# Optimization experiments

Hardware: AMD Instinct MI355X
Metric: run time of the kernel (lower is better)

## Reference

```python
import math
import jax, jax.numpy as jnp
import numpy as np

N_WL = 262144
T_REF = 273.15          # CONSTANTS.STANDARD_TEMPERATURE [K]
P_REF = 101325.0        # CONSTANTS.STANDARD_PRESSURE [Pa]
C_LIGHT = 2.99792458e8  # CONSTANTS.SPEED_OF_LIGHT
K_B = 1.380649e-23      # CONSTANTS.BOLTZMANN
N_AVO = 6.02214076e23   # CONSTANTS.AVOGADRO

# hard-coded line database: [center_wl, strength, width, temp_exp]; rows 0-2 O3, 3-5 H2O, 6-9 CO2
LINES = np.array([
    [254.0, 1.15e-17, 2.0, 0.05], [280.0, 5e-18, 3.0, 0.04], [310.0, 1.9e-19, 2.5, 0.03],
    [940.0, 2.5e-23, 3.0, 0.4],  [1130.0, 8.2e-24, 2.5, 0.35], [1380.0, 1.8e-22, 4.0, 0.45],
    [1400.0, 3.5e-25, 3.0, 0.5], [1600.0, 7.8e-26, 2.5, 0.48], [2000.0, 4.2e-24, 4.0, 0.52],
    [2700.0, 1.2e-24, 3.5, 0.49]], dtype=np.float32)
MASS = np.array([48.0]*3 + [18.0]*3 + [44.0]*4, dtype=np.float32)


def setup_inputs() -> dict:
    key = jax.random.key(0)
    ks = jax.random.split(key, 8)
    inp = {
        'wavelengths': jnp.linspace(200.0, 3000.0, N_WL, dtype=jnp.float32),
        'temperature': jnp.float32(250.0),
        'pressure': jnp.float32(80000.0),
        'conc_o3': jnp.float32(1e-6),
        'conc_h2o': jnp.float32(1e-2),
        'conc_co2': jnp.float32(4e-4),
        'mix_w1': jax.random.normal(ks[0], (10, 64), jnp.float32) * 0.3,
        'mix_b1': jnp.zeros((64,), jnp.float32),
        'mix_w2': jax.random.normal(ks[1], (64, 64), jnp.float32) * 0.12,
        'mix_b2': jnp.zeros((64,), jnp.float32),
        'mix_w3': jax.random.normal(ks[2], (64, N_WL), jnp.float32) * 0.12,
        'mix_b3': jnp.zeros((N_WL,), jnp.float32),
        'cont_w1': jax.random.normal(ks[3], (5, 32), jnp.float32) * 0.4,
        'cont_b1': jnp.zeros((32,), jnp.float32),
        'cont_w2': jax.random.normal(ks[4], (32, N_WL), jnp.float32) * 0.17,
        'cont_b2': jnp.zeros((N_WL,), jnp.float32),
    }
    return inp


def _voigt(wl, nu0, gamma_L, gamma_D):
    # wl: [N]; nu0, gamma_L, gamma_D: [L] -> returns [L, N]
    sigma = gamma_D / (math.sqrt(2.0 * math.log(2.0)) + 1e-12)          # [L]
    x = (wl[None, :] - nu0[:, None]) / (sigma[:, None] + 1e-12)          # [L,N]
    y = (gamma_L / (sigma + 1e-12))[:, None]                             # [L,1]
    t = y - 1j * x
    s = jnp.abs(x) + y
    mask1 = s >= 15.0
    mask2 = (s < 15.0) & (jnp.abs(x) >= 5.5)
    w1 = (t * 0.5641896 / (0.5 + t ** 2)).real
    u = t ** 2
    w2 = (t * (1.410474 + u * 0.5641896) / (0.75 + u * (3.0 + u))).real
    w3 = (jnp.exp(-x ** 2) * jnp.cos(2.0 * x * y) / math.sqrt(math.pi)
          + 2.0 * y / math.pi * jnp.sin(x ** 2) / (x ** 2 + y ** 2 + 1e-10))
    result = jnp.where(mask1, w1, jnp.where(mask2, w2, w3))
    return result / (sigma[:, None] * math.sqrt(math.pi) + 1e-12)


def reference(wavelengths, temperature, pressure, conc_o3, conc_h2o, conc_co2,
              mix_w1, mix_b1, mix_w2, mix_b2, mix_w3, mix_b3,
              cont_w1, cont_b1, cont_w2, cont_b2):
    lines = jnp.asarray(LINES)
    mass = jnp.asarray(MASS)
    conc = jnp.stack([conc_o3, conc_o3, conc_o3,
                      conc_h2o, conc_h2o, conc_h2o,
                      conc_co2, conc_co2, conc_co2, conc_co2])          # [10]
    nu0, strength, width, temp_exp = lines[:, 0], lines[:, 1], lines[:, 2], lines[:, 3]
    strength_T = strength * (T_REF / (temperature + 1e-12)) ** temp_exp  # [10]
    gamma_L = width * (pressure / (P_REF + 1e-12)) * jnp.sqrt(T_REF / (temperature + 1e-12))
    gamma_D = nu0 / C_LIGHT * jnp.sqrt(2.0 * K_B * temperature * N_AVO / (mass + 1e-12))

    profiles = _voigt(wavelengths, nu0, gamma_L, gamma_D)                # [10,N]
    cross = jnp.sum((conc * strength_T)[:, None] * profiles, axis=0)     # [N]

    # continuum net: 5 -> 32 (SiLU) -> N (softplus)
    cont_feat = jnp.stack([temperature / (T_REF + 1e-12),
                           pressure / (P_REF + 1e-12),
                           conc_h2o,
                           jnp.float32(1.0), jnp.float32(0.0)])
    h = jax.nn.silu(cont_feat @ cont_w1 + cont_b1)
    continuum = jax.nn.softplus(h @ cont_w2 + cont_b2)
    cross = cross + continuum

    # line-mixing net: 10 -> 64 (SiLU) -> 64 (SiLU) -> N (sigmoid); dropout is eval-mode identity
    mix_feat = jnp.concatenate([jnp.stack([temperature / (T_REF + 1e-12),
                                           pressure / (P_REF + 1e-12)]),
                                cross[:8]])
    m = jax.nn.silu(mix_feat @ mix_w1 + mix_b1)
    m = jax.nn.silu(m @ mix_w2 + mix_b2)
    mixing = jax.nn.sigmoid(m @ mix_w3 + mix_b3)
    return cross * (1.0 + 0.1 * (mixing - 0.5))
```

## Files before the change

### kernel.cpp

```cpp
#include <hip/hip_runtime.h>
#include <math.h>

#define N_WL 262144

#define T_REF 273.15
#define P_REF 101325.0
#define C_LIGHT 299792458.0
#define K_B 1.380649e-23
#define N_AVO 6.02214076e+23

__constant__ float c_nu0[10]  = {254.0f, 280.0f, 310.0f, 940.0f, 1130.0f, 1380.0f, 1400.0f, 1600.0f, 2000.0f, 2700.0f};
__constant__ float c_str[10]  = {1.15e-17f, 5e-18f, 1.9e-19f, 2.5e-23f, 8.2e-24f, 1.8e-22f, 3.5e-25f, 7.8e-26f, 4.2e-24f, 1.2e-24f};
__constant__ float c_wid[10]  = {2.0f, 3.0f, 2.5f, 3.0f, 2.5f, 4.0f, 3.0f, 2.5f, 4.0f, 3.5f};
__constant__ float c_texp[10] = {0.05f, 0.04f, 0.03f, 0.4f, 0.35f, 0.45f, 0.5f, 0.48f, 0.52f, 0.49f};
__constant__ float c_mass[10] = {48.f, 48.f, 48.f, 18.f, 18.f, 18.f, 44.f, 44.f, 44.f, 44.f};
__constant__ int   c_cidx[10] = {0, 0, 0, 1, 1, 1, 2, 2, 2, 2};

#define WS_M2    0
#define WS_H     64
#define WS_NU0   96
#define WS_ISIG  106
#define WS_Y     116
#define WS_SCALE 126
#define WS_TOT   136

__device__ __forceinline__ float siluf(float x)     { return x / (1.0f + __expf(-x)); }
__device__ __forceinline__ float sigmoidf(float x)  { return 1.0f / (1.0f + __expf(-x)); }
__device__ __forceinline__ float softplusf(float x) { return fmaxf(x, 0.0f) + log1pf(expf(-fabsf(x))); }

__device__ __forceinline__ float voigt_w(float x, float y) {
    float ax = fabsf(x);
    float s  = ax + y;
    if (s >= 15.0f) {
        float ur = y * y - x * x;
        float ui = -2.0f * x * y;
        float dr = 0.5f + ur, di = ui;
        float nr = 0.5641896f * y, ni = 0.5641896f * (-x);
        float den = dr * dr + di * di;
        return (nr * dr + ni * di) / den;
    } else if (ax >= 5.5f) {
        float ur = y * y - x * x;
        float ui = -2.0f * x * y;
        float pr = 1.410474f + 0.5641896f * ur;
        float pi_ = 0.5641896f * ui;
        float tr = y, ti = -x;
        float nr = tr * pr - ti * pi_;
        float ni = tr * pi_ + ti * pr;
        float u2r = ur * ur - ui * ui;
        float u2i = 2.0f * ur * ui;
        float dr = 0.75f + 3.0f * ur + u2r;
        float di = 3.0f * ui + u2i;
        float den = dr * dr + di * di;
        return (nr * dr + ni * di) / den;
    } else {
        float x2 = x * x;
        return expf(-x2) * cosf(2.0f * x * y) * 0.5641895835477563f
             + (2.0f * y / 3.14159265358979f) * sinf(x2) / (x2 + y * y + 1e-10f);
    }
}

__global__ void GasAbs_setup_kernel(
    const float* __restrict__ wl,
    const float* __restrict__ Tp, const float* __restrict__ Pp,
    const float* __restrict__ o3, const float* __restrict__ h2o, const float* __restrict__ co2,
    const float* __restrict__ mix_w1, const float* __restrict__ mix_b1,
    const float* __restrict__ mix_w2, const float* __restrict__ mix_b2,
    const float* __restrict__ cont_w1, const float* __restrict__ cont_b1,
    const float* __restrict__ cont_w2, const float* __restrict__ cont_b2,
    float* __restrict__ ws)
{
    __shared__ float sp[WS_TOT];
    __shared__ float s_feat[10];
    __shared__ float s_m1[64];

    const int t = threadIdx.x;
    const double T = (double)Tp[0];
    const double P = (double)Pp[0];
    const float  cc[3] = {o3[0], h2o[0], co2[0]};

    if (t < 10) {
        double nu0 = (double)c_nu0[t];
        double sT  = (double)c_str[t] * pow(T_REF / (T + 1e-12), (double)c_texp[t]);
        double gL  = (double)c_wid[t] * (P / (P_REF + 1e-12)) * sqrt(T_REF / (T + 1e-12));
        double gD  = nu0 / C_LIGHT * sqrt(2.0 * K_B * T * N_AVO / ((double)c_mass[t] + 1e-12));
        double sig = gD / (sqrt(2.0 * log(2.0)) + 1e-12);
        sp[WS_NU0  + t] = (float)nu0;
        sp[WS_ISIG + t] = (float)(1.0 / (sig + 1e-12));
        sp[WS_Y    + t] = (float)(gL / (sig + 1e-12));
        sp[WS_SCALE+ t] = (float)((double)cc[c_cidx[t]] * sT / (sig * sqrt(M_PI) + 1e-12));
    }
    if (t < 32) {
        float cf[5];
        cf[0] = (float)(T / (T_REF + 1e-12));
        cf[1] = (float)(P / (P_REF + 1e-12));
        cf[2] = cc[1];
        cf[3] = 1.0f;
        cf[4] = 0.0f;
        float a = cont_b1[t];
        #pragma unroll
        for (int k = 0; k < 5; k++) a += cf[k] * cont_w1[k * 32 + t];
        sp[WS_H + t] = siluf(a);
    }
    __syncthreads();

    if (t < 8) {
        float w = wl[t];
        float c = cont_b2[t];
        #pragma unroll
        for (int j = 0; j < 32; j++) c += sp[WS_H + j] * cont_w2[(size_t)j * N_WL + t];
        float cross = softplusf(c);
        #pragma unroll
        for (int l = 0; l < 10; l++) {
            float x = (w - sp[WS_NU0 + l]) * sp[WS_ISIG + l];
            cross += sp[WS_SCALE + l] * voigt_w(x, sp[WS_Y + l]);
        }
        s_feat[2 + t] = cross;
    }
    if (t == 0) {
        s_feat[0] = (float)(T / (T_REF + 1e-12));
        s_feat[1] = (float)(P / (P_REF + 1e-12));
    }
    __syncthreads();

    {
        float a = mix_b1[t];
        #pragma unroll
        for (int k = 0; k < 10; k++) a += s_feat[k] * mix_w1[k * 64 + t];
        s_m1[t] = siluf(a);
    }
    __syncthreads();

    {
        float a = mix_b2[t];
        #pragma unroll
        for (int k = 0; k < 64; k++) a += s_m1[k] * mix_w2[k * 64 + t];
        sp[WS_M2 + t] = siluf(a);
    }
    __syncthreads();

    ws[t] = sp[t];
    if (t < WS_TOT - 64) ws[64 + t] = sp[64 + t];
}

__global__ __launch_bounds__(256) void GasAbs_main_kernel(
    const float* __restrict__ wl,
    const float* __restrict__ mix_w3, const float* __restrict__ mix_b3,
    const float* __restrict__ cont_w2, const float* __restrict__ cont_b2,
    const float* __restrict__ ws,
    float* __restrict__ out)
{
    __shared__ float sp[WS_TOT];
    const int t = threadIdx.x;
    if (t < WS_TOT) sp[t] = ws[t];
    __syncthreads();

    const int i = (blockIdx.x * blockDim.x + t) * 4;
    if (i >= N_WL) return;

    const float4 wlv = *reinterpret_cast<const float4*>(wl + i);

    float4 c = *reinterpret_cast<const float4*>(cont_b2 + i);
    #pragma unroll
    for (int j = 0; j < 32; j++) {
        float hj = sp[WS_H + j];
        float4 w = *reinterpret_cast<const float4*>(cont_w2 + (size_t)j * N_WL + i);
        c.x = fmaf(hj, w.x, c.x);
        c.y = fmaf(hj, w.y, c.y);
        c.z = fmaf(hj, w.z, c.z);
        c.w = fmaf(hj, w.w, c.w);
    }

    float4 cross;
    cross.x = softplusf(c.x);
    cross.y = softplusf(c.y);
    cross.z = softplusf(c.z);
    cross.w = softplusf(c.w);

    #pragma unroll
    for (int l = 0; l < 10; l++) {
        const float nu0 = sp[WS_NU0 + l];
        const float is  = sp[WS_ISIG + l];
        const float y   = sp[WS_Y + l];
        const float sc  = sp[WS_SCALE + l];
        cross.x = fmaf(sc, voigt_w((wlv.x - nu0) * is, y), cross.x);
        cross.y = fmaf(sc, voigt_w((wlv.y - nu0) * is, y), cross.y);
        cross.z = fmaf(sc, voigt_w((wlv.z - nu0) * is, y), cross.z);
        cross.w = fmaf(sc, voigt_w((wlv.w - nu0) * is, y), cross.w);
    }

    float4 m = *reinterpret_cast<const float4*>(mix_b3 + i);
    #pragma unroll
    for (int j = 0; j < 64; j++) {
        float mj = sp[WS_M2 + j];
        float4 w = *reinterpret_cast<const float4*>(mix_w3 + (size_t)j * N_WL + i);
        m.x = fmaf(mj, w.x, m.x);
        m.y = fmaf(mj, w.y, m.y);
        m.z = fmaf(mj, w.z, m.z);
        m.w = fmaf(mj, w.w, m.w);
    }

    float4 o;
    o.x = cross.x * (0.95f + 0.1f * sigmoidf(m.x));
    o.y = cross.y * (0.95f + 0.1f * sigmoidf(m.y));
    o.z = cross.z * (0.95f + 0.1f * sigmoidf(m.z));
    o.w = cross.w * (0.95f + 0.1f * sigmoidf(m.w));
    *reinterpret_cast<float4*>(out + i) = o;
}

extern "C" void kernel_launch(void* const* d_in, const int* in_sizes, int n_in,
                              void* d_out, int out_size, void* d_ws, size_t ws_size,
                              hipStream_t stream) {
    const float* wl      = (const float*)d_in[0];
    const float* Tp      = (const float*)d_in[1];
    const float* Pp      = (const float*)d_in[2];
    const float* o3      = (const float*)d_in[3];
    const float* h2o     = (const float*)d_in[4];
    const float* co2     = (const float*)d_in[5];
    const float* mix_w1  = (const float*)d_in[6];
    const float* mix_b1  = (const float*)d_in[7];
    const float* mix_w2  = (const float*)d_in[8];
    const float* mix_b2  = (const float*)d_in[9];
    const float* mix_w3  = (const float*)d_in[10];
    const float* mix_b3  = (const float*)d_in[11];
    const float* cont_w1 = (const float*)d_in[12];
    const float* cont_b1 = (const float*)d_in[13];
    const float* cont_w2 = (const float*)d_in[14];
    const float* cont_b2 = (const float*)d_in[15];
    float* ws  = (float*)d_ws;
    float* out = (float*)d_out;

    GasAbs_setup_kernel<<<1, 64, 0, stream>>>(
        wl, Tp, Pp, o3, h2o, co2,
        mix_w1, mix_b1, mix_w2, mix_b2,
        cont_w1, cont_b1, cont_w2, cont_b2, ws);

    const int threads = 256;
    const int blocks  = (N_WL / 4 + threads - 1) / threads;
    GasAbs_main_kernel<<<blocks, threads, 0, stream>>>(
        wl, mix_w3, mix_b3, cont_w2, cont_b2, ws, out);
}
```

Baseline: 156.5 us.

## Fuse setup MLP into main kernel, recomputing per block to drop second launch

Merges the single-block setup kernel into the main kernel so that every block recomputes the line parameters, the continuum hidden layer and the two small mixing-MLP layers in shared memory, then proceeds to its per-wavelength work. This removes one kernel launch, the serial dependency between the two kernels and the workspace round trip. In exchange, each of the 256 blocks repeats the setup: double-precision pow/sqrt, 8 Voigt evaluations, and reads of the 64x64 mix_w2 matrix plus a few rows of cont_w2. This adds per-block latency and redundant traffic that mostly hits L2.

```diff
diff --git a/kernel.cpp b/kernel.cpp
--- a/kernel.cpp
+++ b/kernel.cpp
@@ -59,47 +59,54 @@
     }
 }
 
-__global__ void GasAbs_setup_kernel(
+__global__ __launch_bounds__(256) void GasAbs_fused_kernel(
     const float* __restrict__ wl,
     const float* __restrict__ Tp, const float* __restrict__ Pp,
     const float* __restrict__ o3, const float* __restrict__ h2o, const float* __restrict__ co2,
     const float* __restrict__ mix_w1, const float* __restrict__ mix_b1,
     const float* __restrict__ mix_w2, const float* __restrict__ mix_b2,
+    const float* __restrict__ mix_w3, const float* __restrict__ mix_b3,
     const float* __restrict__ cont_w1, const float* __restrict__ cont_b1,
     const float* __restrict__ cont_w2, const float* __restrict__ cont_b2,
-    float* __restrict__ ws)
+    float* __restrict__ out)
 {
     __shared__ float sp[WS_TOT];
     __shared__ float s_feat[10];
     __shared__ float s_m1[64];
 
     const int t = threadIdx.x;
-    const double T = (double)Tp[0];
-    const double P = (double)Pp[0];
-    const float  cc[3] = {o3[0], h2o[0], co2[0]};
-
-    if (t < 10) {
-        double nu0 = (double)c_nu0[t];
-        double sT  = (double)c_str[t] * pow(T_REF / (T + 1e-12), (double)c_texp[t]);
-        double gL  = (double)c_wid[t] * (P / (P_REF + 1e-12)) * sqrt(T_REF / (T + 1e-12));
-        double gD  = nu0 / C_LIGHT * sqrt(2.0 * K_B * T * N_AVO / ((double)c_mass[t] + 1e-12));
-        double sig = gD / (sqrt(2.0 * log(2.0)) + 1e-12);
-        sp[WS_NU0  + t] = (float)nu0;
-        sp[WS_ISIG + t] = (float)(1.0 / (sig + 1e-12));
-        sp[WS_Y    + t] = (float)(gL / (sig + 1e-12));
-        sp[WS_SCALE+ t] = (float)((double)cc[c_cidx[t]] * sT / (sig * sqrt(M_PI) + 1e-12));
-    }
-    if (t < 32) {
-        float cf[5];
-        cf[0] = (float)(T / (T_REF + 1e-12));
-        cf[1] = (float)(P / (P_REF + 1e-12));
-        cf[2] = cc[1];
-        cf[3] = 1.0f;
-        cf[4] = 0.0f;
-        float a = cont_b1[t];
-        #pragma unroll
-        for (int k = 0; k < 5; k++) a += cf[k] * cont_w1[k * 32 + t];
-        sp[WS_H + t] = siluf(a);
+
+    if (t < 64) {
+        const double T = (double)Tp[0];
+        const double P = (double)Pp[0];
+        if (t < 10) {
+            const float cc[3] = {o3[0], h2o[0], co2[0]};
+            double nu0 = (double)c_nu0[t];
+            double sT  = (double)c_str[t] * pow(T_REF / (T + 1e-12), (double)c_texp[t]);
+            double gL  = (double)c_wid[t] * (P / (P_REF + 1e-12)) * sqrt(T_REF / (T + 1e-12));
+            double gD  = nu0 / C_LIGHT * sqrt(2.0 * K_B * T * N_AVO / ((double)c_mass[t] + 1e-12));
+            double sig = gD / (sqrt(2.0 * log(2.0)) + 1e-12);
+            sp[WS_NU0  + t] = (float)nu0;
+            sp[WS_ISIG + t] = (float)(1.0 / (sig + 1e-12));
+            sp[WS_Y    + t] = (float)(gL / (sig + 1e-12));
+            sp[WS_SCALE+ t] = (float)((double)cc[c_cidx[t]] * sT / (sig * sqrt(M_PI) + 1e-12));
+        }
+        if (t < 32) {
+            float cf[5];
+            cf[0] = (float)(T / (T_REF + 1e-12));
+            cf[1] = (float)(P / (P_REF + 1e-12));
+            cf[2] = h2o[0];
+            cf[3] = 1.0f;
+            cf[4] = 0.0f;
+            float a = cont_b1[t];
+            #pragma unroll
+            for (int k = 0; k < 5; k++) a += cf[k] * cont_w1[k * 32 + t];
+            sp[WS_H + t] = siluf(a);
+        }
+        if (t == 0) {
+            s_feat[0] = (float)(T / (T_REF + 1e-12));
+            s_feat[1] = (float)(P / (P_REF + 1e-12));
+        }
     }
     __syncthreads();
 
@@ -116,13 +123,9 @@
         }
         s_feat[2 + t] = cross;
     }
-    if (t == 0) {
-        s_feat[0] = (float)(T / (T_REF + 1e-12));
-        s_feat[1] = (float)(P / (P_REF + 1e-12));
-    }
-    __syncthreads();
-
-    {
+    __syncthreads();
+
+    if (t < 64) {
         float a = mix_b1[t];
         #pragma unroll
         for (int k = 0; k < 10; k++) a += s_feat[k] * mix_w1[k * 64 + t];
@@ -130,7 +133,7 @@
     }
     __syncthreads();
 
-    {
+    if (t < 64) {
         float a = mix_b2[t];
         #pragma unroll
         for (int k = 0; k < 64; k++) a += s_m1[k] * mix_w2[k * 64 + t];
@@ -138,24 +141,7 @@
     }
     __syncthreads();
 
-    ws[t] = sp[t];
-    if (t < WS_TOT - 64) ws[64 + t] = sp[64 + t];
-}
-
-__global__ __launch_bounds__(256) void GasAbs_main_kernel(
-    const float* __restrict__ wl,
-    const float* __restrict__ mix_w3, const float* __restrict__ mix_b3,
-    const float* __restrict__ cont_w2, const float* __restrict__ cont_b2,
-    const float* __restrict__ ws,
-    float* __restrict__ out)
-{
-    __shared__ float sp[WS_TOT];
-    const int t = threadIdx.x;
-    if (t < WS_TOT) sp[t] = ws[t];
-    __syncthreads();
-
-    const int i = (blockIdx.x * blockDim.x + t) * 4;
-    if (i >= N_WL) return;
+    const int i = (blockIdx.x * 256 + t) * 4;
 
     const float4 wlv = *reinterpret_cast<const float4*>(wl + i);
 
@@ -226,16 +212,14 @@
     const float* cont_b1 = (const float*)d_in[13];
     const float* cont_w2 = (const float*)d_in[14];
     const float* cont_b2 = (const float*)d_in[15];
-    float* ws  = (float*)d_ws;
     float* out = (float*)d_out;
 
-    GasAbs_setup_kernel<<<1, 64, 0, stream>>>(
+    const int threads = 256;
+    const int blocks  = N_WL / (threads * 4);
+    GasAbs_fused_kernel<<<blocks, threads, 0, stream>>>(
         wl, Tp, Pp, o3, h2o, co2,
         mix_w1, mix_b1, mix_w2, mix_b2,
-        cont_w1, cont_b1, cont_w2, cont_b2, ws);
-
-    const int threads = 256;
-    const int blocks  = (N_WL / 4 + threads - 1) / threads;
-    GasAbs_main_kernel<<<blocks, threads, 0, stream>>>(
-        wl, mix_w3, mix_b3, cont_w2, cont_b2, ws, out);
+        mix_w3, mix_b3,
+        cont_w1, cont_b1, cont_w2, cont_b2,
+        out);
 }
```

After: 157.4 us. About the same (+0.5%).
